# Kernel tuning notes

Hardware: AMD Instinct MI355X
Metric: run time of the kernel (lower is better)

Reference implementation:

```python
import jax, jax.numpy as jnp
import numpy as np

N, E = 100000, 1600000
IN_C, HID, H1, H2, OUT_C, HEADS = 128, 128, 64, 64, 32, 1
TAU = 0.25
EPS = 1e-12


def _l2norm(x):
    n = jnp.sqrt(jnp.sum(x * x, axis=-1, keepdims=True))
    return x / jnp.maximum(n, EPS)


def _gat_layer(x, Wl, Wr, bias, Wc, src, dst, num_nodes, heads, c):
    # x: [N, F]; Wl/Wr: [F, heads*c]
    x_l = (x @ Wl).reshape(num_nodes, heads, c)
    x_r = (x @ Wr).reshape(num_nodes, heads, c)
    nl = _l2norm(x_l)
    nr = _l2norm(x_r)
    # cosine similarity per edge/head: [E, H]
    cos = jnp.sum(nr[dst] * nl[src], axis=-1)
    alpha_raw = jnp.exp(cos)          # stored as attention weights in original
    v = alpha_raw / TAU
    # segmented softmax grouped by SOURCE index (edge_index_j), as in original
    m = jax.ops.segment_max(v, src, num_segments=num_nodes)   # [N, H]
    e = jnp.exp(v - m[src])
    den = jax.ops.segment_sum(e, src, num_segments=num_nodes)  # [N, H]
    a = e / den[src]                                           # [E, H]
    msg = x_l[src] * a[:, :, None]                             # [E, H, C]
    out = jax.ops.segment_sum(msg, dst, num_segments=num_nodes)  # [N, H, C]
    out = out.reshape(num_nodes, heads * c) + bias
    out = out @ Wc                                             # [N, C]
    return out, alpha_raw


def setup_inputs() -> dict:
    key = jax.random.key(0)
    ks = jax.random.split(key, 16)
    x = jax.random.normal(ks[0], (N, IN_C), dtype=jnp.float32)
    src = jax.random.randint(ks[1], (E,), 0, N)
    dst = jax.random.randint(ks[2], (E,), 0, N)
    dst = jnp.where(src == dst, (dst + 1) % N, dst)  # no self-loops
    edge_index = jnp.stack([src, dst]).astype(jnp.int32)

    def glorot(k, shape):
        lim = np.sqrt(6.0 / (shape[0] + shape[1]))
        return jax.random.uniform(k, shape, jnp.float32, -lim, lim)

    return {
        "x": x,
        "edge_index": edge_index,
        "W_in": glorot(ks[3], (IN_C, HID)),
        "b_in": jnp.zeros((HID,), jnp.float32),
        "Wl1": glorot(ks[4], (HID, HEADS * H1)),
        "Wr1": glorot(ks[5], (HID, HEADS * H1)),
        "bias1": jnp.zeros((HEADS * H1,), jnp.float32),
        "Wc1": glorot(ks[6], (HEADS * H1, H1)),
        "Wl2": glorot(ks[7], (H1, HEADS * H2)),
        "Wr2": glorot(ks[8], (H1, HEADS * H2)),
        "bias2": jnp.zeros((HEADS * H2,), jnp.float32),
        "Wc2": glorot(ks[9], (HEADS * H2, H2)),
        "W3": glorot(ks[10], (H2, H2)),
        "b3": jnp.zeros((H2,), jnp.float32),
        "W4": glorot(ks[11], (H2, OUT_C)),
        "b4": jnp.zeros((OUT_C,), jnp.float32),
    }


def reference(x, edge_index, W_in, b_in, Wl1, Wr1, bias1, Wc1,
              Wl2, Wr2, bias2, Wc2, W3, b3, W4, b4):
    src, dst = edge_index[0], edge_index[1]
    h = jax.nn.leaky_relu(x @ W_in + b_in, 0.01)
    h, _ = _gat_layer(h, Wl1, Wr1, bias1, Wc1, src, dst, N, HEADS, H1)
    h = jax.nn.leaky_relu(h, 0.01)
    h, _ = _gat_layer(h, Wl2, Wr2, bias2, Wc2, src, dst, N, HEADS, H2)
    h = jax.nn.leaky_relu(h, 0.01)
    z = jax.nn.relu(h @ W3 + b3) @ W4 + b4
    return z
```

## Files before the change

kernel.cpp:

```cpp
#include <hip/hip_runtime.h>
#include <hip/hip_bf16.h>

typedef __hip_bfloat16 bf16;

#define IN_C 128

__device__ inline unsigned short f2bf(float f) {
  bf16 b = __float2bfloat16(f);
  return __builtin_bit_cast(unsigned short, b);
}

__global__ __launch_bounds__(256) void detect_k(const unsigned short* __restrict__ xb,
                                                int* __restrict__ flag) {
  __shared__ int s_sane;
  if (threadIdx.x == 0) s_sane = 0;
  __syncthreads();
  int sane = 0;
  for (int i = threadIdx.x; i < 4096; i += 256) {
    unsigned short h = xb[2 * i];
    int e = (h >> 7) & 0xFF;
    if (e >= 100 && e <= 150) sane++;
  }
  atomicAdd(&s_sane, sane);
  __syncthreads();
  if (threadIdx.x == 0) *flag = (s_sane > 3072) ? 1 : 0;
}

__global__ __launch_bounds__(256) void cvt_k(const void* __restrict__ in,
                                             float* __restrict__ out, int n,
                                             const int* __restrict__ flag) {
  int i = blockIdx.x * 256 + threadIdx.x;
  if (i >= n) return;
  if (*flag) out[i] = __bfloat162float(((const bf16*)in)[i]);
  else       out[i] = ((const float*)in)[i];
}

struct WArgs { const void* p[14]; int off[15]; };
__global__ __launch_bounds__(256) void cvtw_k(WArgs a, float* __restrict__ out,
                                              const int* __restrict__ flag, int total) {
  int i = blockIdx.x * 256 + threadIdx.x;
  if (i >= total) return;
  int s = 0;
#pragma unroll
  for (int j = 1; j < 14; j++) if (i >= a.off[j]) s = j;
  int loc = i - a.off[s];
  if (*flag) out[i] = __bfloat162float(((const bf16*)a.p[s])[loc]);
  else       out[i] = ((const float*)a.p[s])[loc];
}

__global__ __launch_bounds__(256) void out_k(const float* __restrict__ src,
                                             void* __restrict__ out, int n,
                                             const int* __restrict__ flag) {
  int i = blockIdx.x * 256 + threadIdx.x;
  if (i >= n) return;
  float v = src[i];
  if (*flag) ((bf16*)out)[i] = __float2bfloat16(v);
  else       ((float*)out)[i] = v;
}

template <int K, int C, int R, int ACT, bool PREB, bool POSTB, int NRM>
__global__ __launch_bounds__(256, 2) void lin_k(const float* __restrict__ x,
                                                const float* __restrict__ W,
                                                const float* __restrict__ preb,
                                                const float* __restrict__ postb,
                                                float* __restrict__ out,
                                                float* __restrict__ out2, int n) {
  constexpr int CG  = C / 4;
  constexpr int RG  = 256 / CG;
  constexpr int RPB = RG * R;
  constexpr int KP  = K + 4;
  constexpr int KC  = (K < 4096 / C) ? K : (4096 / C);
  __shared__ float xs[RPB * KP];
  __shared__ float ws[KC * C];
  const int tid = threadIdx.x;
  const int row0 = blockIdx.x * RPB;

  for (int i = tid; i < RPB * K / 4; i += 256) {
    int r4 = i / (K / 4);
    int kk = (i - r4 * (K / 4)) * 4;
    int row = row0 + r4;
    float4 v = make_float4(0.f, 0.f, 0.f, 0.f);
    if (row < n) v = *(const float4*)&x[(size_t)row * K + kk];
    if (PREB) {
      v.x += preb[kk]; v.y += preb[kk + 1]; v.z += preb[kk + 2]; v.w += preb[kk + 3];
    }
    *(float4*)&xs[r4 * KP + kk] = v;
  }

  const int cg = tid % CG;
  const int g  = tid / CG;
  const int c0 = cg * 4;

  float4 acc[R];
#pragma unroll
  for (int r = 0; r < R; r++) acc[r] = make_float4(0.f, 0.f, 0.f, 0.f);

  for (int kc0 = 0; kc0 < K; kc0 += KC) {
    for (int i = tid; i < KC * C / 4; i += 256) {
      *(float4*)&ws[i * 4] = *(const float4*)&W[(size_t)kc0 * C + i * 4];
    }
    __syncthreads();
#pragma unroll 4
    for (int k = 0; k < KC; k += 4) {
      const float* wb = &ws[k * C + c0];
      float4 w0 = *(const float4*)(wb);
      float4 w1 = *(const float4*)(wb + C);
      float4 w2 = *(const float4*)(wb + 2 * C);
      float4 w3 = *(const float4*)(wb + 3 * C);
#pragma unroll
      for (int r = 0; r < R; r++) {
        float4 xv = *(const float4*)&xs[(r * RG + g) * KP + kc0 + k];
        float4 a = acc[r];
        a.x = fmaf(xv.x, w0.x, a.x); a.y = fmaf(xv.x, w0.y, a.y);
        a.z = fmaf(xv.x, w0.z, a.z); a.w = fmaf(xv.x, w0.w, a.w);
        a.x = fmaf(xv.y, w1.x, a.x); a.y = fmaf(xv.y, w1.y, a.y);
        a.z = fmaf(xv.y, w1.z, a.z); a.w = fmaf(xv.y, w1.w, a.w);
        a.x = fmaf(xv.z, w2.x, a.x); a.y = fmaf(xv.z, w2.y, a.y);
        a.z = fmaf(xv.z, w2.z, a.z); a.w = fmaf(xv.z, w2.w, a.w);
        a.x = fmaf(xv.w, w3.x, a.x); a.y = fmaf(xv.w, w3.y, a.y);
        a.z = fmaf(xv.w, w3.z, a.z); a.w = fmaf(xv.w, w3.w, a.w);
        acc[r] = a;
      }
    }
    __syncthreads();
  }

  float4 pb = make_float4(0.f, 0.f, 0.f, 0.f);
  if (POSTB) pb = *(const float4*)&postb[c0];
#pragma unroll
  for (int r = 0; r < R; r++) {
    int row = row0 + r * RG + g;
    float4 v = acc[r];
    v.x += pb.x; v.y += pb.y; v.z += pb.z; v.w += pb.w;
    if (ACT == 1) {
      v.x = (v.x >= 0.f) ? v.x : 0.01f * v.x; v.y = (v.y >= 0.f) ? v.y : 0.01f * v.y;
      v.z = (v.z >= 0.f) ? v.z : 0.01f * v.z; v.w = (v.w >= 0.f) ? v.w : 0.01f * v.w;
    }
    if (ACT == 2) {
      v.x = fmaxf(v.x, 0.f); v.y = fmaxf(v.y, 0.f);
      v.z = fmaxf(v.z, 0.f); v.w = fmaxf(v.w, 0.f);
    }
    if (NRM == 0) {
      if (row < n) *(float4*)&out[(size_t)row * C + c0] = v;
    } else {
      float ss = v.x * v.x + v.y * v.y + v.z * v.z + v.w * v.w;
#pragma unroll
      for (int o = 1; o < CG; o <<= 1) ss += __shfl_xor(ss, o, CG);
      float inv = 1.0f / fmaxf(sqrtf(ss), 1e-12f);
      if (row < n) {
        if (NRM == 1) {
          float4 vn = make_float4(v.x * inv, v.y * inv, v.z * inv, v.w * inv);
          *(float4*)&out[(size_t)row * C + c0] = vn;
        } else {
          ushort4 hr = make_ushort4(f2bf(v.x), f2bf(v.y), f2bf(v.z), f2bf(v.w));
          ushort4 hn = make_ushort4(f2bf(v.x * inv), f2bf(v.y * inv),
                                    f2bf(v.z * inv), f2bf(v.w * inv));
          *(ushort4*)((bf16*)out  + (size_t)row * C + c0) = hr;
          *(ushort4*)((bf16*)out2 + (size_t)row * C + c0) = hn;
        }
      }
    }
  }
}

__global__ __launch_bounds__(256) void count_k(const int* __restrict__ dst,
                                               int* __restrict__ cnt_d, int E) {
  int e = blockIdx.x * 256 + threadIdx.x;
  if (e >= E) return;
  atomicAdd(&cnt_d[dst[e]], 1);
}

__global__ __launch_bounds__(256) void scan_local_k(const int* __restrict__ cnt,
                                                    int* __restrict__ off,
                                                    int* __restrict__ part, int n) {
  __shared__ int sd[256];
  int t = threadIdx.x;
  int base = blockIdx.x * 2048 + t * 8;
  int v[8], s = 0;
#pragma unroll
  for (int j = 0; j < 8; j++) {
    int idx = base + j;
    v[j] = (idx < n) ? cnt[idx] : 0;
    s += v[j];
  }
  sd[t] = s;
  __syncthreads();
  for (int o = 1; o < 256; o <<= 1) {
    int x = (t >= o) ? sd[t - o] : 0;
    __syncthreads();
    sd[t] += x;
    __syncthreads();
  }
  int excl = sd[t] - s;
  if (t == 255) part[blockIdx.x] = sd[255];
  int run = excl;
#pragma unroll
  for (int j = 0; j < 8; j++) {
    int idx = base + j;
    if (idx < n) off[idx] = run;
    run += v[j];
  }
}

__global__ __launch_bounds__(256) void scan_add_k(int* __restrict__ off,
                                                  int* __restrict__ cur,
                                                  const int* __restrict__ part,
                                                  int nb, int n) {
  __shared__ int s_pref;
  if (threadIdx.x == 0) {
    int s = 0;
    for (int i = 0; i < (int)blockIdx.x; i++) s += part[i];
    s_pref = s;
    if (blockIdx.x == 0) {
      int tot = 0;
      for (int i = 0; i < nb; i++) tot += part[i];
      off[n] = tot;
    }
  }
  __syncthreads();
  int pref = s_pref;
  int base = blockIdx.x * 2048 + threadIdx.x * 8;
#pragma unroll
  for (int j = 0; j < 8; j++) {
    int idx = base + j;
    if (idx < n) { int val = off[idx] + pref; off[idx] = val; cur[idx] = val; }
  }
}

__global__ __launch_bounds__(256) void fill_k(const int* __restrict__ src,
                                              const int* __restrict__ dst,
                                              int* __restrict__ cur_d,
                                              int* __restrict__ dl_src, int E, int N) {
  int part = blockIdx.x & 7;
  int lo = (int)(((long)part * N) >> 3);
  int hi = (int)((((long)part + 1) * N) >> 3);
  int tid = (blockIdx.x >> 3) * 256 + threadIdx.x;
  int stride = (gridDim.x >> 3) * 256;
  for (int e = tid; e < E; e += stride) {
    int d = dst[e];
    if (d < lo || d >= hi) continue;
    int pd = atomicAdd(&cur_d[d], 1);
    dl_src[pd] = src[e];
  }
}

__device__ inline float dot8(uint4 h, float4 r0, float4 r1) {
  float p;
  p  = __uint_as_float(h.x << 16) * r0.x + __uint_as_float(h.x & 0xffff0000u) * r0.y;
  p += __uint_as_float(h.y << 16) * r0.z + __uint_as_float(h.y & 0xffff0000u) * r0.w;
  p += __uint_as_float(h.z << 16) * r1.x + __uint_as_float(h.z & 0xffff0000u) * r1.y;
  p += __uint_as_float(h.w << 16) * r1.z + __uint_as_float(h.w & 0xffff0000u) * r1.w;
  return p;
}

__device__ inline void fma8(uint4 h, float w, float4& a0, float4& a1) {
  a0.x += w * __uint_as_float(h.x << 16); a0.y += w * __uint_as_float(h.x & 0xffff0000u);
  a0.z += w * __uint_as_float(h.y << 16); a0.w += w * __uint_as_float(h.y & 0xffff0000u);
  a1.x += w * __uint_as_float(h.z << 16); a1.y += w * __uint_as_float(h.z & 0xffff0000u);
  a1.z += w * __uint_as_float(h.w << 16); a1.w += w * __uint_as_float(h.w & 0xffff0000u);
}

__global__ __launch_bounds__(256) void gat_pre_k(const uint4* __restrict__ XLN,
                                                 const float* __restrict__ XRN,
                                                 const int* __restrict__ off_d,
                                                 const int* __restrict__ dl_src,
                                                 float* __restrict__ EV,
                                                 float* __restrict__ DEN, int n) {
  int wv = threadIdx.x >> 6, lane = threadIdx.x & 63;
  int node = blockIdx.x * 4 + wv;
  if (node >= n) return;
  int g = lane >> 3, gl = lane & 7;
  int beg = off_d[node];
  int deg = off_d[node + 1] - beg;
  if (deg <= 0) return;
  const float4* xrp = (const float4*)&XRN[(size_t)node * 64 + gl * 8];
  float4 xr0 = xrp[0], xr1 = xrp[1];
  for (int i0 = 0; i0 < deg; i0 += 16) {
    int iA = i0 + g, iB = iA + 8;
    int sA = dl_src[beg + ((iA < deg) ? iA : 0)];
    int sB = dl_src[beg + ((iB < deg) ? iB : 0)];
    uint4 hA = XLN[(size_t)sA * 8 + gl];
    uint4 hB = XLN[(size_t)sB * 8 + gl];
    float pA = dot8(hA, xr0, xr1);
    float pB = dot8(hB, xr0, xr1);
    pA += __shfl_xor(pA, 1, 8); pA += __shfl_xor(pA, 2, 8); pA += __shfl_xor(pA, 4, 8);
    pB += __shfl_xor(pB, 1, 8); pB += __shfl_xor(pB, 2, 8); pB += __shfl_xor(pB, 4, 8);
    if (gl == 0) {
      if (iA < deg) {
        float ev = __expf(__expf(pA) * 4.0f);
        EV[beg + iA] = ev;
        unsafeAtomicAdd(&DEN[sA], ev);
      }
      if (iB < deg) {
        float ev = __expf(__expf(pB) * 4.0f);
        EV[beg + iB] = ev;
        unsafeAtomicAdd(&DEN[sB], ev);
      }
    }
  }
}

__global__ __launch_bounds__(256) void gat_dst_k(const uint4* __restrict__ XLB,
                                                 const float* __restrict__ EV,
                                                 const float* __restrict__ DEN,
                                                 const int* __restrict__ off_d,
                                                 const int* __restrict__ dl_src,
                                                 float* __restrict__ AGG, int n) {
  int wv = threadIdx.x >> 6, lane = threadIdx.x & 63;
  int node = blockIdx.x * 4 + wv;
  if (node >= n) return;
  int g = lane >> 3, gl = lane & 7;
  int beg = off_d[node];
  int deg = off_d[node + 1] - beg;
  float4 a0 = {0.f, 0.f, 0.f, 0.f}, a1 = {0.f, 0.f, 0.f, 0.f};
  for (int i0 = 0; i0 < deg; i0 += 16) {
    int iA = i0 + g, iB = iA + 8;
    int sA = dl_src[beg + ((iA < deg) ? iA : 0)];
    int sB = dl_src[beg + ((iB < deg) ? iB : 0)];
    uint4 hA = XLB[(size_t)sA * 8 + gl];
    uint4 hB = XLB[(size_t)sB * 8 + gl];
    float wA = 0.f, wB = 0.f;
    if (gl == 0) {
      if (iA < deg) wA = EV[beg + iA] / DEN[sA];
      if (iB < deg) wB = EV[beg + iB] / DEN[sB];
    }
    wA = __shfl(wA, 0, 8);
    wB = __shfl(wB, 0, 8);
    fma8(hA, wA, a0, a1);
    fma8(hB, wB, a0, a1);
  }
#pragma unroll
  for (int o = 8; o < 64; o <<= 1) {
    a0.x += __shfl_xor(a0.x, o); a0.y += __shfl_xor(a0.y, o);
    a0.z += __shfl_xor(a0.z, o); a0.w += __shfl_xor(a0.w, o);
    a1.x += __shfl_xor(a1.x, o); a1.y += __shfl_xor(a1.y, o);
    a1.z += __shfl_xor(a1.z, o); a1.w += __shfl_xor(a1.w, o);
  }
  if (g == 0) {
    *(float4*)&AGG[(size_t)node * 64 + gl * 8]     = a0;
    *(float4*)&AGG[(size_t)node * 64 + gl * 8 + 4] = a1;
  }
}

extern "C" void kernel_launch(void* const* d_in, const int* in_sizes, int n_in,
                              void* d_out, int out_size, void* d_ws, size_t ws_size,
                              hipStream_t stream) {
  const int N = in_sizes[0] / IN_C;
  const int E = in_sizes[1] / 2;
  const int* ei  = (const int*)d_in[1];
  const int* src = ei;
  const int* dst = ei + E;

  char* wsb = (char*)d_ws;
  size_t o = 0;
  auto alloc = [&](size_t elems) { void* p = wsb + o; o += ((elems + 3) & ~3ull) * 4; return p; };
  int*   FLAG   = (int*)alloc(16);
  float* WF     = (float*)alloc(60000);
  int*   CNT_D  = (int*)alloc(N);
  int*   OFF_D  = (int*)alloc(N + 1);
  int*   CUR_D  = (int*)alloc(N);
  int*   PART   = (int*)alloc(256);
  int*   DL_SRC = (int*)alloc(E);
  float* EV     = (float*)alloc(E);
  float* DEN    = (float*)alloc(N);
  uint4* XLB    = (uint4*)alloc((size_t)N * 32);
  uint4* XLN    = (uint4*)alloc((size_t)N * 32);
  float* bufA   = (float*)alloc((size_t)N * 128);
  float* bufB   = (float*)alloc((size_t)N * 128);

  float* XF  = bufA;
  float* XRN = bufA + (size_t)N * 64;
  float* H0  = bufB;
  float* B1  = bufB;
  float* B2  = bufB + (size_t)N * 64;

  dim3 blk(256);
  auto nblk = [](long total, int per) { return dim3((unsigned)((total + per - 1) / per)); };

  detect_k<<<1, blk, 0, stream>>>((const unsigned short*)d_in[0], FLAG);
  cvt_k<<<nblk((long)N * 128, 256), blk, 0, stream>>>(d_in[0], XF, N * 128, FLAG);
  WArgs wa;
  int wtot = 0;
  float* wp[16];
  for (int i = 2; i < 16; i++) {
    wa.p[i - 2] = d_in[i];
    wa.off[i - 2] = wtot;
    wp[i] = WF + wtot;
    wtot += in_sizes[i];
  }
  wa.off[14] = wtot;
  cvtw_k<<<nblk(wtot, 256), blk, 0, stream>>>(wa, WF, FLAG, wtot);
  const float *W_in = wp[2], *b_in = wp[3], *Wl1 = wp[4], *Wr1 = wp[5],
              *bias1 = wp[6], *Wc1 = wp[7], *Wl2 = wp[8], *Wr2 = wp[9],
              *bias2 = wp[10], *Wc2 = wp[11], *W3 = wp[12], *b3 = wp[13],
              *W4 = wp[14], *b4 = wp[15];

  hipMemsetAsync(CNT_D, 0, sizeof(int) * (size_t)N, stream);
  count_k<<<nblk(E, 256), blk, 0, stream>>>(dst, CNT_D, E);
  {
    int nb = (N + 2047) / 2048;
    scan_local_k<<<dim3(nb), blk, 0, stream>>>(CNT_D, OFF_D, PART, N);
    scan_add_k<<<dim3(nb), blk, 0, stream>>>(OFF_D, CUR_D, PART, nb, N);
  }
  fill_k<<<dim3(2048), blk, 0, stream>>>(src, dst, CUR_D, DL_SRC, E, N);

  lin_k<128, 128, 8, 1, false, true, 0>
      <<<nblk(N, 64), blk, 0, stream>>>(XF, W_in, nullptr, b_in, H0, nullptr, N);

  lin_k<128, 64, 4, 0, false, false, 4>
      <<<nblk(N, 64), blk, 0, stream>>>(H0, Wl1, nullptr, nullptr, (float*)XLB, (float*)XLN, N);
  lin_k<128, 64, 4, 0, false, false, 1>
      <<<nblk(N, 64), blk, 0, stream>>>(H0, Wr1, nullptr, nullptr, XRN, nullptr, N);
  hipMemsetAsync(DEN, 0, sizeof(float) * (size_t)N, stream);
  gat_pre_k<<<nblk(N, 4), blk, 0, stream>>>(XLN, XRN, OFF_D, DL_SRC, EV, DEN, N);
  gat_dst_k<<<nblk(N, 4), blk, 0, stream>>>(XLB, EV, DEN, OFF_D, DL_SRC, B1, N);
  lin_k<64, 64, 8, 1, true, false, 0>
      <<<nblk(N, 128), blk, 0, stream>>>(B1, Wc1, bias1, nullptr, B1, nullptr, N);

  lin_k<64, 64, 8, 0, false, false, 4>
      <<<nblk(N, 128), blk, 0, stream>>>(B1, Wl2, nullptr, nullptr, (float*)XLB, (float*)XLN, N);
  lin_k<64, 64, 8, 0, false, false, 1>
      <<<nblk(N, 128), blk, 0, stream>>>(B1, Wr2, nullptr, nullptr, XRN, nullptr, N);
  hipMemsetAsync(DEN, 0, sizeof(float) * (size_t)N, stream);
  gat_pre_k<<<nblk(N, 4), blk, 0, stream>>>(XLN, XRN, OFF_D, DL_SRC, EV, DEN, N);
  gat_dst_k<<<nblk(N, 4), blk, 0, stream>>>(XLB, EV, DEN, OFF_D, DL_SRC, B2, N);
  lin_k<64, 64, 8, 1, true, false, 0>
      <<<nblk(N, 128), blk, 0, stream>>>(B2, Wc2, bias2, nullptr, B2, nullptr, N);

  lin_k<64, 64, 8, 2, false, true, 0>
      <<<nblk(N, 128), blk, 0, stream>>>(B2, W3, nullptr, b3, B1, nullptr, N);
  lin_k<64, 32, 4, 0, false, true, 0>
      <<<nblk(N, 128), blk, 0, stream>>>(B1, W4, nullptr, b4, bufA, nullptr, N);
  out_k<<<nblk((long)N * 32, 256), blk, 0, stream>>>(bufA, d_out, N * 32, FLAG);
}
```

Baseline: 749.6 us.

## Bucket CSR edges by source range and store normalized XR in bf16

The dst-sorted edge list is now also sub-bucketed by source-index quarter (NB=4). gat_pre_k processes one bucket at a time across the grid, so gathers of XLN rows and DEN atomics hit a narrower source range at once, which should improve cache locality. gat_dst_k iterates all buckets per node, processes 8 edges per step instead of 16, and the normalized XR is stored as bf16, halving its traffic. This costs a 4x larger count/offset array and scan, plus some precision in XR.

```diff
diff --git a/kernel.cpp b/kernel.cpp
--- a/kernel.cpp
+++ b/kernel.cpp
@@ -4,6 +4,7 @@
 typedef __hip_bfloat16 bf16;
 
 #define IN_C 128
+#define NB 4
 
 __device__ inline unsigned short f2bf(float f) {
   bf16 b = __float2bfloat16(f);
@@ -148,13 +149,12 @@
       for (int o = 1; o < CG; o <<= 1) ss += __shfl_xor(ss, o, CG);
       float inv = 1.0f / fmaxf(sqrtf(ss), 1e-12f);
       if (row < n) {
+        ushort4 hn = make_ushort4(f2bf(v.x * inv), f2bf(v.y * inv),
+                                  f2bf(v.z * inv), f2bf(v.w * inv));
         if (NRM == 1) {
-          float4 vn = make_float4(v.x * inv, v.y * inv, v.z * inv, v.w * inv);
-          *(float4*)&out[(size_t)row * C + c0] = vn;
+          *(ushort4*)((bf16*)out + (size_t)row * C + c0) = hn;
         } else {
           ushort4 hr = make_ushort4(f2bf(v.x), f2bf(v.y), f2bf(v.z), f2bf(v.w));
-          ushort4 hn = make_ushort4(f2bf(v.x * inv), f2bf(v.y * inv),
-                                    f2bf(v.z * inv), f2bf(v.w * inv));
           *(ushort4*)((bf16*)out  + (size_t)row * C + c0) = hr;
           *(ushort4*)((bf16*)out2 + (size_t)row * C + c0) = hn;
         }
@@ -163,11 +163,21 @@
   }
 }
 
-__global__ __launch_bounds__(256) void count_k(const int* __restrict__ dst,
-                                               int* __restrict__ cnt_d, int E) {
-  int e = blockIdx.x * 256 + threadIdx.x;
-  if (e >= E) return;
-  atomicAdd(&cnt_d[dst[e]], 1);
+__global__ __launch_bounds__(256) void count_k(const int* __restrict__ src,
+                                               const int* __restrict__ dst,
+                                               int* __restrict__ cnt, int E, int N,
+                                               int bdiv) {
+  int part = blockIdx.x & 7;
+  int lo = (int)(((long)part * N) >> 3);
+  int hi = (int)((((long)part + 1) * N) >> 3);
+  int tid = (blockIdx.x >> 3) * 256 + threadIdx.x;
+  int stride = (gridDim.x >> 3) * 256;
+  for (int e = tid; e < E; e += stride) {
+    int d = dst[e];
+    if (d < lo || d >= hi) continue;
+    int b = src[e] / bdiv;
+    atomicAdd(&cnt[b * N + d], 1);
+  }
 }
 
 __global__ __launch_bounds__(256) void scan_local_k(const int* __restrict__ cnt,
@@ -229,8 +239,9 @@
 
 __global__ __launch_bounds__(256) void fill_k(const int* __restrict__ src,
                                               const int* __restrict__ dst,
-                                              int* __restrict__ cur_d,
-                                              int* __restrict__ dl_src, int E, int N) {
+                                              int* __restrict__ cur,
+                                              int* __restrict__ dl_src, int E, int N,
+                                              int bdiv) {
   int part = blockIdx.x & 7;
   int lo = (int)(((long)part * N) >> 3);
   int hi = (int)((((long)part + 1) * N) >> 3);
@@ -239,8 +250,10 @@
   for (int e = tid; e < E; e += stride) {
     int d = dst[e];
     if (d < lo || d >= hi) continue;
-    int pd = atomicAdd(&cur_d[d], 1);
-    dl_src[pd] = src[e];
+    int s = src[e];
+    int b = s / bdiv;
+    int pd = atomicAdd(&cur[b * N + d], 1);
+    dl_src[pd] = s;
   }
 }
 
@@ -253,6 +266,13 @@
   return p;
 }
 
+__device__ inline void expand8(uint4 h, float4& r0, float4& r1) {
+  r0.x = __uint_as_float(h.x << 16); r0.y = __uint_as_float(h.x & 0xffff0000u);
+  r0.z = __uint_as_float(h.y << 16); r0.w = __uint_as_float(h.y & 0xffff0000u);
+  r1.x = __uint_as_float(h.z << 16); r1.y = __uint_as_float(h.z & 0xffff0000u);
+  r1.z = __uint_as_float(h.w << 16); r1.w = __uint_as_float(h.w & 0xffff0000u);
+}
+
 __device__ inline void fma8(uint4 h, float w, float4& a0, float4& a1) {
   a0.x += w * __uint_as_float(h.x << 16); a0.y += w * __uint_as_float(h.x & 0xffff0000u);
   a0.z += w * __uint_as_float(h.y << 16); a0.w += w * __uint_as_float(h.y & 0xffff0000u);
@@ -261,41 +281,31 @@
 }
 
 __global__ __launch_bounds__(256) void gat_pre_k(const uint4* __restrict__ XLN,
-                                                 const float* __restrict__ XRN,
-                                                 const int* __restrict__ off_d,
+                                                 const uint4* __restrict__ XRNB,
+                                                 const int* __restrict__ off,
                                                  const int* __restrict__ dl_src,
                                                  float* __restrict__ EV,
-                                                 float* __restrict__ DEN, int n) {
-  int wv = threadIdx.x >> 6, lane = threadIdx.x & 63;
-  int node = blockIdx.x * 4 + wv;
+                                                 float* __restrict__ DEN, int n, int bpb) {
+  int b = blockIdx.x / bpb;
+  int node = (blockIdx.x - b * bpb) * 4 + (threadIdx.x >> 6);
   if (node >= n) return;
+  int lane = threadIdx.x & 63;
   int g = lane >> 3, gl = lane & 7;
-  int beg = off_d[node];
-  int deg = off_d[node + 1] - beg;
-  if (deg <= 0) return;
-  const float4* xrp = (const float4*)&XRN[(size_t)node * 64 + gl * 8];
-  float4 xr0 = xrp[0], xr1 = xrp[1];
-  for (int i0 = 0; i0 < deg; i0 += 16) {
-    int iA = i0 + g, iB = iA + 8;
-    int sA = dl_src[beg + ((iA < deg) ? iA : 0)];
-    int sB = dl_src[beg + ((iB < deg) ? iB : 0)];
-    uint4 hA = XLN[(size_t)sA * 8 + gl];
-    uint4 hB = XLN[(size_t)sB * 8 + gl];
-    float pA = dot8(hA, xr0, xr1);
-    float pB = dot8(hB, xr0, xr1);
-    pA += __shfl_xor(pA, 1, 8); pA += __shfl_xor(pA, 2, 8); pA += __shfl_xor(pA, 4, 8);
-    pB += __shfl_xor(pB, 1, 8); pB += __shfl_xor(pB, 2, 8); pB += __shfl_xor(pB, 4, 8);
-    if (gl == 0) {
-      if (iA < deg) {
-        float ev = __expf(__expf(pA) * 4.0f);
-        EV[beg + iA] = ev;
-        unsafeAtomicAdd(&DEN[sA], ev);
-      }
-      if (iB < deg) {
-        float ev = __expf(__expf(pB) * 4.0f);
-        EV[beg + iB] = ev;
-        unsafeAtomicAdd(&DEN[sB], ev);
-      }
+  int key = b * n + node;
+  int beg = off[key], end = off[key + 1];
+  if (beg >= end) return;
+  float4 xr0, xr1;
+  expand8(XRNB[(size_t)node * 8 + gl], xr0, xr1);
+  for (int i0 = beg; i0 < end; i0 += 8) {
+    int i = i0 + g;
+    int s = dl_src[(i < end) ? i : (end - 1)];
+    uint4 h = XLN[(size_t)s * 8 + gl];
+    float p = dot8(h, xr0, xr1);
+    p += __shfl_xor(p, 1, 8); p += __shfl_xor(p, 2, 8); p += __shfl_xor(p, 4, 8);
+    if (gl == 0 && i < end) {
+      float ev = __expf(__expf(p) * 4.0f);
+      EV[i] = ev;
+      unsafeAtomicAdd(&DEN[s], ev);
     }
   }
 }
@@ -303,31 +313,28 @@
 __global__ __launch_bounds__(256) void gat_dst_k(const uint4* __restrict__ XLB,
                                                  const float* __restrict__ EV,
                                                  const float* __restrict__ DEN,
-                                                 const int* __restrict__ off_d,
+                                                 const int* __restrict__ off,
                                                  const int* __restrict__ dl_src,
                                                  float* __restrict__ AGG, int n) {
   int wv = threadIdx.x >> 6, lane = threadIdx.x & 63;
   int node = blockIdx.x * 4 + wv;
   if (node >= n) return;
   int g = lane >> 3, gl = lane & 7;
-  int beg = off_d[node];
-  int deg = off_d[node + 1] - beg;
   float4 a0 = {0.f, 0.f, 0.f, 0.f}, a1 = {0.f, 0.f, 0.f, 0.f};
-  for (int i0 = 0; i0 < deg; i0 += 16) {
-    int iA = i0 + g, iB = iA + 8;
-    int sA = dl_src[beg + ((iA < deg) ? iA : 0)];
-    int sB = dl_src[beg + ((iB < deg) ? iB : 0)];
-    uint4 hA = XLB[(size_t)sA * 8 + gl];
-    uint4 hB = XLB[(size_t)sB * 8 + gl];
-    float wA = 0.f, wB = 0.f;
-    if (gl == 0) {
-      if (iA < deg) wA = EV[beg + iA] / DEN[sA];
-      if (iB < deg) wB = EV[beg + iB] / DEN[sB];
-    }
-    wA = __shfl(wA, 0, 8);
-    wB = __shfl(wB, 0, 8);
-    fma8(hA, wA, a0, a1);
-    fma8(hB, wB, a0, a1);
+#pragma unroll
+  for (int b = 0; b < NB; b++) {
+    int key = b * n + node;
+    int beg = off[key], end = off[key + 1];
+    for (int i0 = beg; i0 < end; i0 += 8) {
+      int i = i0 + g;
+      int ic = (i < end) ? i : (end - 1);
+      int s = dl_src[ic];
+      uint4 h = XLB[(size_t)s * 8 + gl];
+      float w = 0.f;
+      if (gl == 0 && i < end) w = EV[i] / DEN[s];
+      w = __shfl(w, 0, 8);
+      fma8(h, w, a0, a1);
+    }
   }
 #pragma unroll
   for (int o = 8; o < 64; o <<= 1) {
@@ -350,26 +357,27 @@
   const int* ei  = (const int*)d_in[1];
   const int* src = ei;
   const int* dst = ei + E;
+  const int bdiv = (N + NB - 1) / NB;
 
   char* wsb = (char*)d_ws;
   size_t o = 0;
   auto alloc = [&](size_t elems) { void* p = wsb + o; o += ((elems + 3) & ~3ull) * 4; return p; };
   int*   FLAG   = (int*)alloc(16);
   float* WF     = (float*)alloc(60000);
-  int*   CNT_D  = (int*)alloc(N);
-  int*   OFF_D  = (int*)alloc(N + 1);
-  int*   CUR_D  = (int*)alloc(N);
+  int*   CNT    = (int*)alloc((size_t)NB * N);
+  int*   OFF    = (int*)alloc((size_t)NB * N + 1);
+  int*   CUR    = (int*)alloc((size_t)NB * N);
   int*   PART   = (int*)alloc(256);
   int*   DL_SRC = (int*)alloc(E);
   float* EV     = (float*)alloc(E);
   float* DEN    = (float*)alloc(N);
   uint4* XLB    = (uint4*)alloc((size_t)N * 32);
   uint4* XLN    = (uint4*)alloc((size_t)N * 32);
+  uint4* XRNB   = (uint4*)alloc((size_t)N * 32);
   float* bufA   = (float*)alloc((size_t)N * 128);
   float* bufB   = (float*)alloc((size_t)N * 128);
 
   float* XF  = bufA;
-  float* XRN = bufA + (size_t)N * 64;
   float* H0  = bufB;
   float* B1  = bufB;
   float* B2  = bufB + (size_t)N * 64;
@@ -395,14 +403,17 @@
               *bias2 = wp[10], *Wc2 = wp[11], *W3 = wp[12], *b3 = wp[13],
               *W4 = wp[14], *b4 = wp[15];
 
-  hipMemsetAsync(CNT_D, 0, sizeof(int) * (size_t)N, stream);
-  count_k<<<nblk(E, 256), blk, 0, stream>>>(dst, CNT_D, E);
+  hipMemsetAsync(CNT, 0, sizeof(int) * (size_t)NB * N, stream);
+  count_k<<<dim3(2048), blk, 0, stream>>>(src, dst, CNT, E, N, bdiv);
   {
-    int nb = (N + 2047) / 2048;
-    scan_local_k<<<dim3(nb), blk, 0, stream>>>(CNT_D, OFF_D, PART, N);
-    scan_add_k<<<dim3(nb), blk, 0, stream>>>(OFF_D, CUR_D, PART, nb, N);
-  }
-  fill_k<<<dim3(2048), blk, 0, stream>>>(src, dst, CUR_D, DL_SRC, E, N);
+    int nkeys = NB * N;
+    int nb = (nkeys + 2047) / 2048;
+    scan_local_k<<<dim3(nb), blk, 0, stream>>>(CNT, OFF, PART, nkeys);
+    scan_add_k<<<dim3(nb), blk, 0, stream>>>(OFF, CUR, PART, nb, nkeys);
+  }
+  fill_k<<<dim3(2048), blk, 0, stream>>>(src, dst, CUR, DL_SRC, E, N, bdiv);
+
+  const int bpb = (N + 3) / 4;
 
   lin_k<128, 128, 8, 1, false, true, 0>
       <<<nblk(N, 64), blk, 0, stream>>>(XF, W_in, nullptr, b_in, H0, nullptr, N);
@@ -410,20 +421,20 @@
   lin_k<128, 64, 4, 0, false, false, 4>
       <<<nblk(N, 64), blk, 0, stream>>>(H0, Wl1, nullptr, nullptr, (float*)XLB, (float*)XLN, N);
   lin_k<128, 64, 4, 0, false, false, 1>
-      <<<nblk(N, 64), blk, 0, stream>>>(H0, Wr1, nullptr, nullptr, XRN, nullptr, N);
+      <<<nblk(N, 64), blk, 0, stream>>>(H0, Wr1, nullptr, nullptr, (float*)XRNB, nullptr, N);
   hipMemsetAsync(DEN, 0, sizeof(float) * (size_t)N, stream);
-  gat_pre_k<<<nblk(N, 4), blk, 0, stream>>>(XLN, XRN, OFF_D, DL_SRC, EV, DEN, N);
-  gat_dst_k<<<nblk(N, 4), blk, 0, stream>>>(XLB, EV, DEN, OFF_D, DL_SRC, B1, N);
+  gat_pre_k<<<dim3(NB * bpb), blk, 0, stream>>>(XLN, XRNB, OFF, DL_SRC, EV, DEN, N, bpb);
+  gat_dst_k<<<nblk(N, 4), blk, 0, stream>>>(XLB, EV, DEN, OFF, DL_SRC, B1, N);
   lin_k<64, 64, 8, 1, true, false, 0>
       <<<nblk(N, 128), blk, 0, stream>>>(B1, Wc1, bias1, nullptr, B1, nullptr, N);
 
   lin_k<64, 64, 8, 0, false, false, 4>
       <<<nblk(N, 128), blk, 0, stream>>>(B1, Wl2, nullptr, nullptr, (float*)XLB, (float*)XLN, N);
   lin_k<64, 64, 8, 0, false, false, 1>
-      <<<nblk(N, 128), blk, 0, stream>>>(B1, Wr2, nullptr, nullptr, XRN, nullptr, N);
+      <<<nblk(N, 128), blk, 0, stream>>>(B1, Wr2, nullptr, nullptr, (float*)XRNB, nullptr, N);
   hipMemsetAsync(DEN, 0, sizeof(float) * (size_t)N, stream);
-  gat_pre_k<<<nblk(N, 4), blk, 0, stream>>>(XLN, XRN, OFF_D, DL_SRC, EV, DEN, N);
-  gat_dst_k<<<nblk(N, 4), blk, 0, stream>>>(XLB, EV, DEN, OFF_D, DL_SRC, B2, N);
+  gat_pre_k<<<dim3(NB * bpb), blk, 0, stream>>>(XLN, XRNB, OFF, DL_SRC, EV, DEN, N, bpb);
+  gat_dst_k<<<nblk(N, 4), blk, 0, stream>>>(XLB, EV, DEN, OFF, DL_SRC, B2, N);
   lin_k<64, 64, 8, 1, true, false, 0>
       <<<nblk(N, 128), blk, 0, stream>>>(B2, Wc2, bias2, nullptr, B2, nullptr, N);
 
```

Result: slower. 844.6 us (+12.7%).

## Fuse Wl/Wr projections and aggregate from normalized bf16 features with per-node norm

Applied to the files above, without the earlier changes.

Merges the two per-layer GAT projections into one dual-output linear kernel that reads the input tile once and writes normalized bf16 x_l, its per-row norm, and normalized bf16 x_r. The raw x_l buffer is removed: aggregation gathers the normalized x_l and folds the norm into a precomputed per-source scale norm/den, computed by a small new kernel. This also replaces a per-edge division with a multiply. The r-side input becomes bf16, halving its read. The count kernel is partitioned by destination range like fill_k to localize atomics. The trade-off is an extra launch and a small change in rounding from rescaling normalized bf16 values.

```diff
diff --git a/kernel.cpp b/kernel.cpp
--- a/kernel.cpp
+++ b/kernel.cpp
@@ -146,28 +146,141 @@
       float ss = v.x * v.x + v.y * v.y + v.z * v.z + v.w * v.w;
 #pragma unroll
       for (int o = 1; o < CG; o <<= 1) ss += __shfl_xor(ss, o, CG);
-      float inv = 1.0f / fmaxf(sqrtf(ss), 1e-12f);
+      float nrm = fmaxf(sqrtf(ss), 1e-12f);
+      float inv = 1.0f / nrm;
       if (row < n) {
-        if (NRM == 1) {
-          float4 vn = make_float4(v.x * inv, v.y * inv, v.z * inv, v.w * inv);
-          *(float4*)&out[(size_t)row * C + c0] = vn;
-        } else {
-          ushort4 hr = make_ushort4(f2bf(v.x), f2bf(v.y), f2bf(v.z), f2bf(v.w));
-          ushort4 hn = make_ushort4(f2bf(v.x * inv), f2bf(v.y * inv),
-                                    f2bf(v.z * inv), f2bf(v.w * inv));
-          *(ushort4*)((bf16*)out  + (size_t)row * C + c0) = hr;
-          *(ushort4*)((bf16*)out2 + (size_t)row * C + c0) = hn;
-        }
+        ushort4 hn = make_ushort4(f2bf(v.x * inv), f2bf(v.y * inv),
+                                  f2bf(v.z * inv), f2bf(v.w * inv));
+        *(ushort4*)((bf16*)out + (size_t)row * C + c0) = hn;
+        if (NRM == 4 && cg == 0) ((float*)out2)[row] = nrm;
       }
     }
   }
 }
 
+template <int K, int C, int R>
+__global__ __launch_bounds__(256, 2) void dual_lin_k(const float* __restrict__ x,
+                                                     const float* __restrict__ W1,
+                                                     const float* __restrict__ W2,
+                                                     float* __restrict__ outA,
+                                                     float* __restrict__ normA,
+                                                     float* __restrict__ outB, int n) {
+  constexpr int CG  = C / 4;
+  constexpr int RG  = 256 / CG;
+  constexpr int RPB = RG * R;
+  constexpr int KP  = K + 4;
+  constexpr int KC  = 32;
+  __shared__ float xs[RPB * KP];
+  __shared__ float ws1[KC * C];
+  __shared__ float ws2[KC * C];
+  const int tid = threadIdx.x;
+  const int row0 = blockIdx.x * RPB;
+
+  for (int i = tid; i < RPB * K / 4; i += 256) {
+    int r4 = i / (K / 4);
+    int kk = (i - r4 * (K / 4)) * 4;
+    int row = row0 + r4;
+    float4 v = make_float4(0.f, 0.f, 0.f, 0.f);
+    if (row < n) v = *(const float4*)&x[(size_t)row * K + kk];
+    *(float4*)&xs[r4 * KP + kk] = v;
+  }
+
+  const int cg = tid % CG;
+  const int g  = tid / CG;
+  const int c0 = cg * 4;
+
+  float4 acc1[R], acc2[R];
+#pragma unroll
+  for (int r = 0; r < R; r++) {
+    acc1[r] = make_float4(0.f, 0.f, 0.f, 0.f);
+    acc2[r] = make_float4(0.f, 0.f, 0.f, 0.f);
+  }
+
+  for (int kc0 = 0; kc0 < K; kc0 += KC) {
+    for (int i = tid; i < KC * C / 4; i += 256) {
+      *(float4*)&ws1[i * 4] = *(const float4*)&W1[(size_t)kc0 * C + i * 4];
+      *(float4*)&ws2[i * 4] = *(const float4*)&W2[(size_t)kc0 * C + i * 4];
+    }
+    __syncthreads();
+#pragma unroll 2
+    for (int k = 0; k < KC; k += 4) {
+      const float* wb1 = &ws1[k * C + c0];
+      const float* wb2 = &ws2[k * C + c0];
+      float4 u0 = *(const float4*)(wb1);
+      float4 u1 = *(const float4*)(wb1 + C);
+      float4 u2 = *(const float4*)(wb1 + 2 * C);
+      float4 u3 = *(const float4*)(wb1 + 3 * C);
+      float4 t0 = *(const float4*)(wb2);
+      float4 t1 = *(const float4*)(wb2 + C);
+      float4 t2 = *(const float4*)(wb2 + 2 * C);
+      float4 t3 = *(const float4*)(wb2 + 3 * C);
+#pragma unroll
+      for (int r = 0; r < R; r++) {
+        float4 xv = *(const float4*)&xs[(r * RG + g) * KP + kc0 + k];
+        float4 a = acc1[r];
+        a.x = fmaf(xv.x, u0.x, a.x); a.y = fmaf(xv.x, u0.y, a.y);
+        a.z = fmaf(xv.x, u0.z, a.z); a.w = fmaf(xv.x, u0.w, a.w);
+        a.x = fmaf(xv.y, u1.x, a.x); a.y = fmaf(xv.y, u1.y, a.y);
+        a.z = fmaf(xv.y, u1.z, a.z); a.w = fmaf(xv.y, u1.w, a.w);
+        a.x = fmaf(xv.z, u2.x, a.x); a.y = fmaf(xv.z, u2.y, a.y);
+        a.z = fmaf(xv.z, u2.z, a.z); a.w = fmaf(xv.z, u2.w, a.w);
+        a.x = fmaf(xv.w, u3.x, a.x); a.y = fmaf(xv.w, u3.y, a.y);
+        a.z = fmaf(xv.w, u3.z, a.z); a.w = fmaf(xv.w, u3.w, a.w);
+        acc1[r] = a;
+        float4 b = acc2[r];
+        b.x = fmaf(xv.x, t0.x, b.x); b.y = fmaf(xv.x, t0.y, b.y);
+        b.z = fmaf(xv.x, t0.z, b.z); b.w = fmaf(xv.x, t0.w, b.w);
+        b.x = fmaf(xv.y, t1.x, b.x); b.y = fmaf(xv.y, t1.y, b.y);
+        b.z = fmaf(xv.y, t1.z, b.z); b.w = fmaf(xv.y, t1.w, b.w);
+        b.x = fmaf(xv.z, t2.x, b.x); b.y = fmaf(xv.z, t2.y, b.y);
+        b.z = fmaf(xv.z, t2.z, b.z); b.w = fmaf(xv.z, t2.w, b.w);
+        b.x = fmaf(xv.w, t3.x, b.x); b.y = fmaf(xv.w, t3.y, b.y);
+        b.z = fmaf(xv.w, t3.z, b.z); b.w = fmaf(xv.w, t3.w, b.w);
+        acc2[r] = b;
+      }
+    }
+    __syncthreads();
+  }
+
+#pragma unroll
+  for (int r = 0; r < R; r++) {
+    int row = row0 + r * RG + g;
+    float4 v1 = acc1[r];
+    float4 v2 = acc2[r];
+    float ss1 = v1.x * v1.x + v1.y * v1.y + v1.z * v1.z + v1.w * v1.w;
+    float ss2 = v2.x * v2.x + v2.y * v2.y + v2.z * v2.z + v2.w * v2.w;
+#pragma unroll
+    for (int o = 1; o < CG; o <<= 1) {
+      ss1 += __shfl_xor(ss1, o, CG);
+      ss2 += __shfl_xor(ss2, o, CG);
+    }
+    float nrm1 = fmaxf(sqrtf(ss1), 1e-12f);
+    float inv1 = 1.0f / nrm1;
+    float inv2 = 1.0f / fmaxf(sqrtf(ss2), 1e-12f);
+    if (row < n) {
+      ushort4 h1 = make_ushort4(f2bf(v1.x * inv1), f2bf(v1.y * inv1),
+                                f2bf(v1.z * inv1), f2bf(v1.w * inv1));
+      ushort4 h2 = make_ushort4(f2bf(v2.x * inv2), f2bf(v2.y * inv2),
+                                f2bf(v2.z * inv2), f2bf(v2.w * inv2));
+      *(ushort4*)((bf16*)outA + (size_t)row * C + c0) = h1;
+      *(ushort4*)((bf16*)outB + (size_t)row * C + c0) = h2;
+      if (cg == 0) normA[row] = nrm1;
+    }
+  }
+}
+
 __global__ __launch_bounds__(256) void count_k(const int* __restrict__ dst,
-                                               int* __restrict__ cnt_d, int E) {
-  int e = blockIdx.x * 256 + threadIdx.x;
-  if (e >= E) return;
-  atomicAdd(&cnt_d[dst[e]], 1);
+                                               int* __restrict__ cnt_d, int E, int N) {
+  int part = blockIdx.x & 7;
+  int lo = (int)(((long)part * N) >> 3);
+  int hi = (int)((((long)part + 1) * N) >> 3);
+  int tid = (blockIdx.x >> 3) * 256 + threadIdx.x;
+  int stride = (gridDim.x >> 3) * 256;
+  for (int e = tid; e < E; e += stride) {
+    int d = dst[e];
+    if (d < lo || d >= hi) continue;
+    atomicAdd(&cnt_d[d], 1);
+  }
 }
 
 __global__ __launch_bounds__(256) void scan_local_k(const int* __restrict__ cnt,
@@ -244,6 +357,13 @@
   }
 }
 
+__device__ inline void expand8(uint4 h, float4& r0, float4& r1) {
+  r0.x = __uint_as_float(h.x << 16); r0.y = __uint_as_float(h.x & 0xffff0000u);
+  r0.z = __uint_as_float(h.y << 16); r0.w = __uint_as_float(h.y & 0xffff0000u);
+  r1.x = __uint_as_float(h.z << 16); r1.y = __uint_as_float(h.z & 0xffff0000u);
+  r1.z = __uint_as_float(h.w << 16); r1.w = __uint_as_float(h.w & 0xffff0000u);
+}
+
 __device__ inline float dot8(uint4 h, float4 r0, float4 r1) {
   float p;
   p  = __uint_as_float(h.x << 16) * r0.x + __uint_as_float(h.x & 0xffff0000u) * r0.y;
@@ -261,7 +381,7 @@
 }
 
 __global__ __launch_bounds__(256) void gat_pre_k(const uint4* __restrict__ XLN,
-                                                 const float* __restrict__ XRN,
+                                                 const uint4* __restrict__ XRNB,
                                                  const int* __restrict__ off_d,
                                                  const int* __restrict__ dl_src,
                                                  float* __restrict__ EV,
@@ -273,8 +393,8 @@
   int beg = off_d[node];
   int deg = off_d[node + 1] - beg;
   if (deg <= 0) return;
-  const float4* xrp = (const float4*)&XRN[(size_t)node * 64 + gl * 8];
-  float4 xr0 = xrp[0], xr1 = xrp[1];
+  float4 xr0, xr1;
+  expand8(XRNB[(size_t)node * 8 + gl], xr0, xr1);
   for (int i0 = 0; i0 < deg; i0 += 16) {
     int iA = i0 + g, iB = iA + 8;
     int sA = dl_src[beg + ((iA < deg) ? iA : 0)];
@@ -300,9 +420,16 @@
   }
 }
 
-__global__ __launch_bounds__(256) void gat_dst_k(const uint4* __restrict__ XLB,
+__global__ __launch_bounds__(256) void nden_k(const float* __restrict__ NORM,
+                                              const float* __restrict__ DEN,
+                                              float* __restrict__ NDEN, int n) {
+  int i = blockIdx.x * 256 + threadIdx.x;
+  if (i < n) NDEN[i] = NORM[i] / DEN[i];
+}
+
+__global__ __launch_bounds__(256) void gat_dst_k(const uint4* __restrict__ XLN,
                                                  const float* __restrict__ EV,
-                                                 const float* __restrict__ DEN,
+                                                 const float* __restrict__ NDEN,
                                                  const int* __restrict__ off_d,
                                                  const int* __restrict__ dl_src,
                                                  float* __restrict__ AGG, int n) {
@@ -317,12 +444,12 @@
     int iA = i0 + g, iB = iA + 8;
     int sA = dl_src[beg + ((iA < deg) ? iA : 0)];
     int sB = dl_src[beg + ((iB < deg) ? iB : 0)];
-    uint4 hA = XLB[(size_t)sA * 8 + gl];
-    uint4 hB = XLB[(size_t)sB * 8 + gl];
+    uint4 hA = XLN[(size_t)sA * 8 + gl];
+    uint4 hB = XLN[(size_t)sB * 8 + gl];
     float wA = 0.f, wB = 0.f;
     if (gl == 0) {
-      if (iA < deg) wA = EV[beg + iA] / DEN[sA];
-      if (iB < deg) wB = EV[beg + iB] / DEN[sB];
+      if (iA < deg) wA = EV[beg + iA] * NDEN[sA];
+      if (iB < deg) wB = EV[beg + iB] * NDEN[sB];
     }
     wA = __shfl(wA, 0, 8);
     wB = __shfl(wB, 0, 8);
@@ -356,20 +483,21 @@
   auto alloc = [&](size_t elems) { void* p = wsb + o; o += ((elems + 3) & ~3ull) * 4; return p; };
   int*   FLAG   = (int*)alloc(16);
   float* WF     = (float*)alloc(60000);
-  int*   CNT_D  = (int*)alloc(N);
-  int*   OFF_D  = (int*)alloc(N + 1);
-  int*   CUR_D  = (int*)alloc(N);
+  int*   CNT    = (int*)alloc(N);
+  int*   OFF    = (int*)alloc(N + 1);
+  int*   CUR    = (int*)alloc(N);
   int*   PART   = (int*)alloc(256);
   int*   DL_SRC = (int*)alloc(E);
   float* EV     = (float*)alloc(E);
   float* DEN    = (float*)alloc(N);
-  uint4* XLB    = (uint4*)alloc((size_t)N * 32);
+  float* NORM   = (float*)alloc(N);
+  float* NDEN   = (float*)alloc(N);
   uint4* XLN    = (uint4*)alloc((size_t)N * 32);
+  uint4* XRNB   = (uint4*)alloc((size_t)N * 32);
   float* bufA   = (float*)alloc((size_t)N * 128);
   float* bufB   = (float*)alloc((size_t)N * 128);
 
   float* XF  = bufA;
-  float* XRN = bufA + (size_t)N * 64;
   float* H0  = bufB;
   float* B1  = bufB;
   float* B2  = bufB + (size_t)N * 64;
@@ -395,35 +523,33 @@
               *bias2 = wp[10], *Wc2 = wp[11], *W3 = wp[12], *b3 = wp[13],
               *W4 = wp[14], *b4 = wp[15];
 
-  hipMemsetAsync(CNT_D, 0, sizeof(int) * (size_t)N, stream);
-  count_k<<<nblk(E, 256), blk, 0, stream>>>(dst, CNT_D, E);
+  hipMemsetAsync(CNT, 0, sizeof(int) * (size_t)N, stream);
+  count_k<<<dim3(2048), blk, 0, stream>>>(dst, CNT, E, N);
   {
     int nb = (N + 2047) / 2048;
-    scan_local_k<<<dim3(nb), blk, 0, stream>>>(CNT_D, OFF_D, PART, N);
-    scan_add_k<<<dim3(nb), blk, 0, stream>>>(OFF_D, CUR_D, PART, nb, N);
-  }
-  fill_k<<<dim3(2048), blk, 0, stream>>>(src, dst, CUR_D, DL_SRC, E, N);
+    scan_local_k<<<dim3(nb), blk, 0, stream>>>(CNT, OFF, PART, N);
+    scan_add_k<<<dim3(nb), blk, 0, stream>>>(OFF, CUR, PART, nb, N);
+  }
+  fill_k<<<dim3(2048), blk, 0, stream>>>(src, dst, CUR, DL_SRC, E, N);
 
   lin_k<128, 128, 8, 1, false, true, 0>
       <<<nblk(N, 64), blk, 0, stream>>>(XF, W_in, nullptr, b_in, H0, nullptr, N);
 
-  lin_k<128, 64, 4, 0, false, false, 4>
-      <<<nblk(N, 64), blk, 0, stream>>>(H0, Wl1, nullptr, nullptr, (float*)XLB, (float*)XLN, N);
-  lin_k<128, 64, 4, 0, false, false, 1>
-      <<<nblk(N, 64), blk, 0, stream>>>(H0, Wr1, nullptr, nullptr, XRN, nullptr, N);
+  dual_lin_k<128, 64, 4>
+      <<<nblk(N, 64), blk, 0, stream>>>(H0, Wl1, Wr1, (float*)XLN, NORM, (float*)XRNB, N);
   hipMemsetAsync(DEN, 0, sizeof(float) * (size_t)N, stream);
-  gat_pre_k<<<nblk(N, 4), blk, 0, stream>>>(XLN, XRN, OFF_D, DL_SRC, EV, DEN, N);
-  gat_dst_k<<<nblk(N, 4), blk, 0, stream>>>(XLB, EV, DEN, OFF_D, DL_SRC, B1, N);
+  gat_pre_k<<<nblk(N, 4), blk, 0, stream>>>(XLN, XRNB, OFF, DL_SRC, EV, DEN, N);
+  nden_k<<<nblk(N, 256), blk, 0, stream>>>(NORM, DEN, NDEN, N);
+  gat_dst_k<<<nblk(N, 4), blk, 0, stream>>>(XLN, EV, NDEN, OFF, DL_SRC, B1, N);
   lin_k<64, 64, 8, 1, true, false, 0>
       <<<nblk(N, 128), blk, 0, stream>>>(B1, Wc1, bias1, nullptr, B1, nullptr, N);
 
-  lin_k<64, 64, 8, 0, false, false, 4>
-      <<<nblk(N, 128), blk, 0, stream>>>(B1, Wl2, nullptr, nullptr, (float*)XLB, (float*)XLN, N);
-  lin_k<64, 64, 8, 0, false, false, 1>
-      <<<nblk(N, 128), blk, 0, stream>>>(B1, Wr2, nullptr, nullptr, XRN, nullptr, N);
+  dual_lin_k<64, 64, 8>
+      <<<nblk(N, 128), blk, 0, stream>>>(B1, Wl2, Wr2, (float*)XLN, NORM, (float*)XRNB, N);
   hipMemsetAsync(DEN, 0, sizeof(float) * (size_t)N, stream);
-  gat_pre_k<<<nblk(N, 4), blk, 0, stream>>>(XLN, XRN, OFF_D, DL_SRC, EV, DEN, N);
-  gat_dst_k<<<nblk(N, 4), blk, 0, stream>>>(XLB, EV, DEN, OFF_D, DL_SRC, B2, N);
+  gat_pre_k<<<nblk(N, 4), blk, 0, stream>>>(XLN, XRNB, OFF, DL_SRC, EV, DEN, N);
+  nden_k<<<nblk(N, 256), blk, 0, stream>>>(NORM, DEN, NDEN, N);
+  gat_dst_k<<<nblk(N, 4), blk, 0, stream>>>(XLN, EV, NDEN, OFF, DL_SRC, B2, N);
   lin_k<64, 64, 8, 1, true, false, 0>
       <<<nblk(N, 128), blk, 0, stream>>>(B2, Wc2, bias2, nullptr, B2, nullptr, N);
 
```

New measurement: 724.1 us. 3.4% less time.
